# Kernel tuning notes

Measured on AMD Instinct MI355X. Metric: run time of the kernel, lower is better.

Reference implementation:

```python
import jax, jax.numpy as jnp
import numpy as np
import math

DROPOUT_P = 0.1

def setup_inputs() -> dict:
    key = jax.random.key(0)
    k1, k2, k3 = jax.random.split(key, 3)
    B, Lq, Lk, D = 8, 2048, 2048, 128
    x1 = jax.random.normal(k1, (B, Lq, D), dtype=jnp.float32)
    x2 = jax.random.normal(k2, (B, Lk, D), dtype=jnp.float32)
    qm = jnp.zeros((1, Lq, Lk), dtype=jnp.float32)  # additive attention mask
    u = jax.random.uniform(k3, (B, Lq, Lk), dtype=jnp.float32)  # dropout uniforms
    return {"x1": x1, "x2": x2, "qm": qm, "u": u}

def reference(x1, x2, qm, u):
    # scaled dot-product attention with additive mask + inverted dropout
    scale = 1.0 / math.sqrt(x1.shape[-1])
    qk = jnp.einsum('bqd,bkd->bqk', x1, x2) * scale + qm  # [B, Lq, Lk]
    attn = jax.nn.softmax(qk, axis=-1)
    keep = (u >= DROPOUT_P).astype(attn.dtype) / (1.0 - DROPOUT_P)
    attn = attn * keep
    out = jnp.einsum('bqk,bkd->bqd', attn, x2)  # [B, Lq, D]
    return out
```

## Files before the change

kernel.cpp:

```cpp
#include <hip/hip_runtime.h>
#include <hip/hip_bf16.h>
#include <stdint.h>

#define LQ 2048
#define LK 2048
#define DH 128
#define BQ 32
#define NT 16
#define LOG2E 1.44269504088896340736f
#define QSCALE 0.088388347648318447f

typedef __attribute__((ext_vector_type(8)))  short bf16x8;
typedef __attribute__((ext_vector_type(16))) float f32x16;
typedef __attribute__((ext_vector_type(4)))  float f32x4;

union FragAB { uint32_t u[4]; bf16x8 v; };

__device__ __forceinline__ uint32_t pack2_bf16(float lo, float hi) {
  union { __hip_bfloat16 b; uint16_t u; } a, c;
  a.b = __float2bfloat16(lo);
  c.b = __float2bfloat16(hi);
  return (uint32_t)a.u | ((uint32_t)c.u << 16);
}

__global__ __launch_bounds__(256)
void prep_kernel(const float* __restrict__ x2, uint16_t* __restrict__ Kp,
                 uint16_t* __restrict__ Vp) {
  __shared__ uint16_t tl[128][130];
  const int b = blockIdx.x & 7, tile = blockIdx.x >> 3;
  const int t = threadIdx.x;
  const int row0 = t >> 1, half = t & 1;

  const float* src = x2 + ((size_t)(b * 2048 + tile * 128 + row0)) * 128 + half * 64;
  uint32_t wbuf[32];
#pragma unroll
  for (int i = 0; i < 16; ++i) {
    f32x4 v = *(const f32x4*)(src + i * 4);
    wbuf[2 * i]     = pack2_bf16(v.x, v.y);
    wbuf[2 * i + 1] = pack2_bf16(v.z, v.w);
  }
  uint16_t* kdst = Kp + ((size_t)(b * 2048 + tile * 128 + row0)) * 128 + half * 64;
#pragma unroll
  for (int i = 0; i < 8; ++i)
    *(uint4*)(kdst + i * 8) = *(const uint4*)&wbuf[i * 4];
#pragma unroll
  for (int i = 0; i < 32; ++i)
    *(uint32_t*)&tl[row0][half * 64 + 2 * i] = wbuf[i];
  __syncthreads();

  const int d = t >> 1, halfk = t & 1;
  uint32_t vw[32];
#pragma unroll
  for (int i = 0; i < 32; ++i) {
    const int k = halfk * 64 + 2 * i;
    vw[i] = (uint32_t)tl[k][d] | ((uint32_t)tl[k + 1][d] << 16);
  }
  uint16_t* vdst = Vp + ((size_t)(b * 128 + d)) * 2048 + tile * 128 + halfk * 64;
#pragma unroll
  for (int i = 0; i < 8; ++i)
    *(uint4*)(vdst + i * 8) = *(const uint4*)&vw[i * 4];
}

__global__ __launch_bounds__(256)
void qmt_kernel(const float* __restrict__ qm, uint16_t* __restrict__ qmt2) {
  const int kc = threadIdx.x & 63;
  const int q  = blockIdx.x * 4 + (threadIdx.x >> 6);
  f32x4 r[8];
  const float* src = qm + (size_t)q * 2048 + kc * 32;
#pragma unroll
  for (int c = 0; c < 8; ++c) r[c] = *(const f32x4*)(src + c * 4);
#pragma unroll
  for (int h = 0; h < 2; ++h) {
    uint32_t w[8];
#pragma unroll
    for (int i = 0; i < 8; ++i) {
      const int gi0 = 2 * i, gi1 = 2 * i + 1;
      const float v0 = r[h + (gi0 >> 2) * 2][gi0 & 3] * LOG2E;
      const float v1 = r[h + (gi1 >> 2) * 2][gi1 & 3] * LOG2E;
      w[i] = pack2_bf16(v0, v1);
    }
    uint16_t* dst = qmt2 + ((size_t)(kc * 2 + h) * 2048 + q) * 16;
    uint4 lo = {w[0], w[1], w[2], w[3]};
    uint4 hi = {w[4], w[5], w[6], w[7]};
    *(uint4*)dst = lo;
    *(uint4*)(dst + 8) = hi;
  }
}

__global__ __launch_bounds__(256, 2)
void fattn_kernel(const float* __restrict__ x1,
                  const uint16_t* __restrict__ Kp,
                  const uint16_t* __restrict__ Vp,
                  const float* __restrict__ uu,
                  const uint16_t* __restrict__ qmt2,
                  float* __restrict__ out)
{
  __shared__ float scr[4][4224];

  const int tid  = threadIdx.x;
  const int ks   = tid >> 6;
  const int lane = tid & 63;
  const int ln   = lane & 31;
  const int h    = lane >> 5;

  const int b     = blockIdx.x & 7;
  const int qblk  = blockIdx.x >> 3;
  const int qbase = qblk * BQ;
  const int qrow  = qbase + ln;

  FragAB qf[8];
  {
    const float* qp = x1 + ((size_t)(b * LQ + qrow)) * DH + h * 8;
    const float qs = QSCALE * LOG2E;
#pragma unroll
    for (int dc = 0; dc < 8; ++dc) {
      f32x4 a = *(const f32x4*)(qp + dc * 16);
      f32x4 c = *(const f32x4*)(qp + dc * 16 + 4);
      qf[dc].u[0] = pack2_bf16(a.x * qs, a.y * qs);
      qf[dc].u[1] = pack2_bf16(a.z * qs, a.w * qs);
      qf[dc].u[2] = pack2_bf16(c.x * qs, c.y * qs);
      qf[dc].u[3] = pack2_bf16(c.z * qs, c.w * qs);
    }
  }

  const uint16_t* Kb = Kp + (size_t)(b * 2048 + ks * 512) * 128;
  const uint16_t* Vb = Vp + (size_t)b * 128 * 2048 + ks * 512;
  const float*    ub = uu + ((size_t)(b * LQ + qbase + h)) * LK + ks * 512 + ln;

  float ucur[16];
#pragma unroll
  for (int i = 0; i < 16; ++i)
    ucur[i] = __builtin_nontemporal_load(ub + (size_t)(2 * i) * LK);

  uint4 qc0, qc1;
  {
    const uint16_t* qp16 = qmt2 + (((size_t)(ks * 16) * 2 + h) * 2048 + qrow) * 16;
    qc0 = *(const uint4*)qp16;
    qc1 = *(const uint4*)(qp16 + 8);
  }

  float m_run = -1e30f, l_run = 0.f;
  f32x16 acco[4];
#pragma unroll
  for (int d2 = 0; d2 < 4; ++d2)
#pragma unroll
    for (int i = 0; i < 16; ++i) acco[d2][i] = 0.f;

  for (int t = 0; t < NT; ++t) {
    const uint16_t* Krow = Kb + (size_t)(t * 32 + ln) * 128 + h * 8;
    bf16x8 kf[8];
#pragma unroll
    for (int dc = 0; dc < 8; ++dc)
      kf[dc] = *(const bf16x8*)(Krow + dc * 16);

    bf16x8 vf[8];
#pragma unroll
    for (int d2 = 0; d2 < 4; ++d2)
#pragma unroll
      for (int c = 0; c < 2; ++c)
        vf[d2 * 2 + c] = *(const bf16x8*)(Vb + (size_t)(d2 * 32 + ln) * 2048 +
                                          t * 32 + c * 16 + h * 8);

    float unxt[16]; uint4 qn0, qn1;
    if (t + 1 < NT) {
#pragma unroll
      for (int i = 0; i < 16; ++i)
        unxt[i] = __builtin_nontemporal_load(ub + (t + 1) * 32 + (size_t)(2 * i) * LK);
      const uint16_t* qp16 = qmt2 + (((size_t)(ks * 16 + t + 1) * 2 + h) * 2048 + qrow) * 16;
      qn0 = *(const uint4*)qp16;
      qn1 = *(const uint4*)(qp16 + 8);
    }

    f32x16 sacc;
#pragma unroll
    for (int i = 0; i < 16; ++i) sacc[i] = 0.f;
    __builtin_amdgcn_s_setprio(1);
#pragma unroll
    for (int dc = 0; dc < 8; ++dc)
      sacc = __builtin_amdgcn_mfma_f32_32x32x16_bf16(kf[dc], qf[dc].v, sacc, 0, 0, 0);
    __builtin_amdgcn_s_setprio(0);

#define ADDQM(W, I) { sacc[I] += __uint_as_float((W) << 16); \
                      sacc[I + 1] += __uint_as_float((W) & 0xffff0000u); }
    ADDQM(qc0.x, 0)  ADDQM(qc0.y, 2)  ADDQM(qc0.z, 4)  ADDQM(qc0.w, 6)
    ADDQM(qc1.x, 8)  ADDQM(qc1.y, 10) ADDQM(qc1.z, 12) ADDQM(qc1.w, 14)
#undef ADDQM

    float pm = sacc[0];
#pragma unroll
    for (int i = 1; i < 16; ++i) pm = fmaxf(pm, sacc[i]);
    pm = fmaxf(pm, __shfl_xor(pm, 32));
    if (!__all(pm <= m_run + 8.f)) {
      const float mnew = fmaxf(m_run, pm);
      const float resc = __builtin_amdgcn_exp2f(m_run - mnew);
      l_run *= resc;
#pragma unroll
      for (int d2 = 0; d2 < 4; ++d2)
#pragma unroll
        for (int i = 0; i < 16; ++i) acco[d2][i] *= resc;
      m_run = mnew;
    }
    float rs = 0.f;
#pragma unroll
    for (int i = 0; i < 16; ++i) {
      sacc[i] = __builtin_amdgcn_exp2f(sacc[i] - m_run);
      rs += sacc[i];
    }
    rs += __shfl_xor(rs, 32);
    l_run += rs;

    uint32_t M = 0;
#pragma unroll
    for (int i = 0; i < 16; ++i) {
      unsigned long long bi = __ballot(ucur[i] >= 0.1f);
      uint32_t sel = (ln & 1) ? (uint32_t)(bi >> 32) : (uint32_t)bi;
      M = ((ln >> 1) == i) ? sel : M;
    }
#pragma unroll
    for (int g = 0; g < 4; ++g)
#pragma unroll
      for (int j2 = 0; j2 < 4; ++j2) {
        const uint32_t keep = (M >> (h * 4 + g * 8 + j2)) & 1u;
        sacc[g * 4 + j2] = keep ? sacc[g * 4 + j2] : 0.f;
      }

    uint32_t pr[4][2], sw[4][2];
#pragma unroll
    for (int g = 0; g < 4; ++g) {
      pr[g][0] = pack2_bf16(sacc[4 * g + 0], sacc[4 * g + 1]);
      pr[g][1] = pack2_bf16(sacc[4 * g + 2], sacc[4 * g + 3]);
      sw[g][0] = __shfl_xor(pr[g][0], 32);
      sw[g][1] = __shfl_xor(pr[g][1], 32);
    }
    FragAB bfr[2];
#pragma unroll
    for (int c = 0; c < 2; ++c) {
      bfr[c].u[0] = h ? sw[2 * c + 1][0] : pr[2 * c][0];
      bfr[c].u[1] = h ? sw[2 * c + 1][1] : pr[2 * c][1];
      bfr[c].u[2] = h ? pr[2 * c + 1][0] : sw[2 * c][0];
      bfr[c].u[3] = h ? pr[2 * c + 1][1] : sw[2 * c][1];
    }

    __builtin_amdgcn_s_setprio(1);
#pragma unroll
    for (int d2 = 0; d2 < 4; ++d2)
#pragma unroll
      for (int c = 0; c < 2; ++c)
        acco[d2] = __builtin_amdgcn_mfma_f32_32x32x16_bf16(vf[d2 * 2 + c], bfr[c].v,
                                                           acco[d2], 0, 0, 0);
    __builtin_amdgcn_s_setprio(0);

    if (t + 1 < NT) {
#pragma unroll
      for (int i = 0; i < 16; ++i) ucur[i] = unxt[i];
      qc0 = qn0; qc1 = qn1;
    }
  }

  float* s = scr[ks];
  s[lane]      = m_run;
  s[64 + lane] = l_run;
#pragma unroll
  for (int d2 = 0; d2 < 4; ++d2)
#pragma unroll
    for (int g = 0; g < 4; ++g) {
      f32x4 vv;
#pragma unroll
      for (int j2 = 0; j2 < 4; ++j2) vv[j2] = acco[d2][g * 4 + j2];
      *(f32x4*)(s + 128 + (size_t)(d2 * 4 + g) * 256 + lane * 4) = vv;
    }
  __syncthreads();

  {
    const float ms0 = scr[0][lane], ms1 = scr[1][lane];
    const float ms2 = scr[2][lane], ms3 = scr[3][lane];
    const float ls0 = scr[0][64 + lane], ls1 = scr[1][64 + lane];
    const float ls2 = scr[2][64 + lane], ls3 = scr[3][64 + lane];
    const float mM = fmaxf(fmaxf(ms0, ms1), fmaxf(ms2, ms3));
    const float e0 = __builtin_amdgcn_exp2f(ms0 - mM);
    const float e1 = __builtin_amdgcn_exp2f(ms1 - mM);
    const float e2 = __builtin_amdgcn_exp2f(ms2 - mM);
    const float e3 = __builtin_amdgcn_exp2f(ms3 - mM);
    const float lM = e0 * ls0 + e1 * ls1 + e2 * ls2 + e3 * ls3;
    const float inv = (1.0f / 0.9f) / lM;
    float* op = out + ((size_t)(b * LQ + qbase + ln)) * DH;
    const int d2 = ks;
#pragma unroll
    for (int g = 0; g < 4; ++g) {
      const size_t off = 128 + (size_t)(d2 * 4 + g) * 256 + lane * 4;
      f32x4 a4 = e0 * *(const f32x4*)(scr[0] + off)
               + e1 * *(const f32x4*)(scr[1] + off)
               + e2 * *(const f32x4*)(scr[2] + off)
               + e3 * *(const f32x4*)(scr[3] + off);
      a4 = a4 * inv;
      *(f32x4*)(op + d2 * 32 + 8 * g + 4 * h) = a4;
    }
  }
}

extern "C" void kernel_launch(void* const* d_in, const int* in_sizes, int n_in,
                              void* d_out, int out_size, void* d_ws, size_t ws_size,
                              hipStream_t stream) {
  (void)in_sizes; (void)n_in; (void)out_size; (void)ws_size;
  const float* x1 = (const float*)d_in[0];
  const float* x2 = (const float*)d_in[1];
  const float* qm = (const float*)d_in[2];
  const float* u  = (const float*)d_in[3];
  float* out = (float*)d_out;

  uint16_t* qmt2 = (uint16_t*)d_ws;
  uint16_t* Kp   = (uint16_t*)((char*)d_ws + (8u  << 20));
  uint16_t* Vp   = (uint16_t*)((char*)d_ws + (12u << 20));

  prep_kernel<<<dim3(128), dim3(256), 0, stream>>>(x2, Kp, Vp);
  qmt_kernel<<<dim3(512), dim3(256), 0, stream>>>(qm, qmt2);
  fattn_kernel<<<dim3(512), dim3(256), 0, stream>>>(x1, Kp, Vp, u, qmt2, out);
}
```

Measured before the change: 273.0 us.

## Precompute dropout keep-bitmasks into LDS with coalesced loads, shrink merge scratch

Before the main loop, each wave streams its 32x512 slice of dropout uniforms with coalesced 16-byte loads and ballots them into packed bitmasks stored in LDS. Per tile, the mask is rebuilt from LDS with bit-spreading, which replaces the per-tile strided scalar loads, register prefetch buffers and per-tile ballots. The cross-wave merge scratch is cut roughly in half and done in two rounds with extra barriers, lowering LDS use, presumably so more blocks fit per CU. The cost is an upfront load phase that is not overlapped with compute, plus extra synchronisation during the merge.

```diff
diff --git a/kernel.cpp b/kernel.cpp
--- a/kernel.cpp
+++ b/kernel.cpp
@@ -21,6 +21,13 @@
   a.b = __float2bfloat16(lo);
   c.b = __float2bfloat16(hi);
   return (uint32_t)a.u | ((uint32_t)c.u << 16);
+}
+
+__device__ __forceinline__ uint32_t spread4(uint32_t x) {
+  x = (x | (x << 12)) & 0x000F000Fu;
+  x = (x | (x << 6))  & 0x03030303u;
+  x = (x | (x << 3))  & 0x11111111u;
+  return x;
 }
 
 __global__ __launch_bounds__(256)
@@ -95,7 +102,9 @@
                   const uint16_t* __restrict__ qmt2,
                   float* __restrict__ out)
 {
-  __shared__ float scr[4][4224];
+  __shared__ uint32_t balLds[4 * 32 * 18];
+  __shared__ float    ml[2][4][64];
+  __shared__ f32x4    mscr[4][2][4][64];
 
   const int tid  = threadIdx.x;
   const int ks   = tid >> 6;
@@ -107,6 +116,28 @@
   const int qblk  = blockIdx.x >> 3;
   const int qbase = qblk * BQ;
   const int qrow  = qbase + ln;
+
+  uint32_t* bal = balLds + ks * 32 * 18;
+  {
+    const float* up0 = uu + ((size_t)(b * 2048 + qbase)) * 2048 + ks * 512;
+#pragma unroll 2
+    for (int r = 0; r < 32; ++r) {
+      const float* rp = up0 + (size_t)r * 2048;
+#pragma unroll
+      for (int cw = 0; cw < 2; ++cw) {
+        f32x4 v = __builtin_nontemporal_load((const f32x4*)(rp + cw * 256 + lane * 4));
+        unsigned long long b0 = __ballot(v.x >= 0.1f);
+        unsigned long long b1 = __ballot(v.y >= 0.1f);
+        unsigned long long b2 = __ballot(v.z >= 0.1f);
+        unsigned long long b3 = __ballot(v.w >= 0.1f);
+        if (lane < 4) {
+          unsigned long long bb = (lane == 0) ? b0 : (lane == 1) ? b1
+                                : (lane == 2) ? b2 : b3;
+          *(unsigned long long*)(bal + r * 18 + cw * 8 + lane * 2) = bb;
+        }
+      }
+    }
+  }
 
   FragAB qf[8];
   {
@@ -125,12 +156,6 @@
 
   const uint16_t* Kb = Kp + (size_t)(b * 2048 + ks * 512) * 128;
   const uint16_t* Vb = Vp + (size_t)b * 128 * 2048 + ks * 512;
-  const float*    ub = uu + ((size_t)(b * LQ + qbase + h)) * LK + ks * 512 + ln;
-
-  float ucur[16];
-#pragma unroll
-  for (int i = 0; i < 16; ++i)
-    ucur[i] = __builtin_nontemporal_load(ub + (size_t)(2 * i) * LK);
 
   uint4 qc0, qc1;
   {
@@ -161,11 +186,22 @@
         vf[d2 * 2 + c] = *(const bf16x8*)(Vb + (size_t)(d2 * 32 + ln) * 2048 +
                                           t * 32 + c * 16 + h * 8);
 
-    float unxt[16]; uint4 qn0, qn1;
+    uint32_t M;
+    {
+      const int cw = t >> 3, L0 = (t & 7) * 8;
+      const uint32_t* bp = bal + ln * 18 + cw * 8;
+      unsigned long long B0 = *(const unsigned long long*)(bp + 0);
+      unsigned long long B1 = *(const unsigned long long*)(bp + 2);
+      unsigned long long B2 = *(const unsigned long long*)(bp + 4);
+      unsigned long long B3 = *(const unsigned long long*)(bp + 6);
+      M = spread4((uint32_t)(B0 >> L0) & 0xFFu)
+        | (spread4((uint32_t)(B1 >> L0) & 0xFFu) << 1)
+        | (spread4((uint32_t)(B2 >> L0) & 0xFFu) << 2)
+        | (spread4((uint32_t)(B3 >> L0) & 0xFFu) << 3);
+    }
+
+    uint4 qn0, qn1;
     if (t + 1 < NT) {
-#pragma unroll
-      for (int i = 0; i < 16; ++i)
-        unxt[i] = __builtin_nontemporal_load(ub + (t + 1) * 32 + (size_t)(2 * i) * LK);
       const uint16_t* qp16 = qmt2 + (((size_t)(ks * 16 + t + 1) * 2 + h) * 2048 + qrow) * 16;
       qn0 = *(const uint4*)qp16;
       qn1 = *(const uint4*)(qp16 + 8);
@@ -209,13 +245,6 @@
     rs += __shfl_xor(rs, 32);
     l_run += rs;
 
-    uint32_t M = 0;
-#pragma unroll
-    for (int i = 0; i < 16; ++i) {
-      unsigned long long bi = __ballot(ucur[i] >= 0.1f);
-      uint32_t sel = (ln & 1) ? (uint32_t)(bi >> 32) : (uint32_t)bi;
-      M = ((ln >> 1) == i) ? sel : M;
-    }
 #pragma unroll
     for (int g = 0; g < 4; ++g)
 #pragma unroll
@@ -250,48 +279,62 @@
                                                            acco[d2], 0, 0, 0);
     __builtin_amdgcn_s_setprio(0);
 
-    if (t + 1 < NT) {
-#pragma unroll
-      for (int i = 0; i < 16; ++i) ucur[i] = unxt[i];
-      qc0 = qn0; qc1 = qn1;
-    }
-  }
-
-  float* s = scr[ks];
-  s[lane]      = m_run;
-  s[64 + lane] = l_run;
-#pragma unroll
-  for (int d2 = 0; d2 < 4; ++d2)
+    if (t + 1 < NT) { qc0 = qn0; qc1 = qn1; }
+  }
+
+  ml[0][ks][lane] = m_run;
+  ml[1][ks][lane] = l_run;
+#pragma unroll
+  for (int dd = 0; dd < 2; ++dd)
 #pragma unroll
     for (int g = 0; g < 4; ++g) {
       f32x4 vv;
 #pragma unroll
-      for (int j2 = 0; j2 < 4; ++j2) vv[j2] = acco[d2][g * 4 + j2];
-      *(f32x4*)(s + 128 + (size_t)(d2 * 4 + g) * 256 + lane * 4) = vv;
+      for (int j2 = 0; j2 < 4; ++j2) vv[j2] = acco[dd][g * 4 + j2];
+      mscr[ks][dd][g][lane] = vv;
     }
   __syncthreads();
 
+  float e0, e1, e2, e3, inv;
   {
-    const float ms0 = scr[0][lane], ms1 = scr[1][lane];
-    const float ms2 = scr[2][lane], ms3 = scr[3][lane];
-    const float ls0 = scr[0][64 + lane], ls1 = scr[1][64 + lane];
-    const float ls2 = scr[2][64 + lane], ls3 = scr[3][64 + lane];
+    const float ms0 = ml[0][0][lane], ms1 = ml[0][1][lane];
+    const float ms2 = ml[0][2][lane], ms3 = ml[0][3][lane];
+    const float ls0 = ml[1][0][lane], ls1 = ml[1][1][lane];
+    const float ls2 = ml[1][2][lane], ls3 = ml[1][3][lane];
     const float mM = fmaxf(fmaxf(ms0, ms1), fmaxf(ms2, ms3));
-    const float e0 = __builtin_amdgcn_exp2f(ms0 - mM);
-    const float e1 = __builtin_amdgcn_exp2f(ms1 - mM);
-    const float e2 = __builtin_amdgcn_exp2f(ms2 - mM);
-    const float e3 = __builtin_amdgcn_exp2f(ms3 - mM);
+    e0 = __builtin_amdgcn_exp2f(ms0 - mM);
+    e1 = __builtin_amdgcn_exp2f(ms1 - mM);
+    e2 = __builtin_amdgcn_exp2f(ms2 - mM);
+    e3 = __builtin_amdgcn_exp2f(ms3 - mM);
     const float lM = e0 * ls0 + e1 * ls1 + e2 * ls2 + e3 * ls3;
-    const float inv = (1.0f / 0.9f) / lM;
-    float* op = out + ((size_t)(b * LQ + qbase + ln)) * DH;
-    const int d2 = ks;
-#pragma unroll
-    for (int g = 0; g < 4; ++g) {
-      const size_t off = 128 + (size_t)(d2 * 4 + g) * 256 + lane * 4;
-      f32x4 a4 = e0 * *(const f32x4*)(scr[0] + off)
-               + e1 * *(const f32x4*)(scr[1] + off)
-               + e2 * *(const f32x4*)(scr[2] + off)
-               + e3 * *(const f32x4*)(scr[3] + off);
+    inv = (1.0f / 0.9f) / lM;
+  }
+
+  float* op = out + ((size_t)(b * LQ + qbase + ln)) * DH;
+  const int mydd = ks & 1;
+  const int g0   = (ks >> 1) * 2;
+
+#pragma unroll
+  for (int r = 0; r < 2; ++r) {
+    if (r == 1) {
+      __syncthreads();
+#pragma unroll
+      for (int dd = 0; dd < 2; ++dd)
+#pragma unroll
+        for (int g = 0; g < 4; ++g) {
+          f32x4 vv;
+#pragma unroll
+          for (int j2 = 0; j2 < 4; ++j2) vv[j2] = acco[2 + dd][g * 4 + j2];
+          mscr[ks][dd][g][lane] = vv;
+        }
+      __syncthreads();
+    }
+    const int d2 = 2 * r + mydd;
+#pragma unroll
+    for (int gi = 0; gi < 2; ++gi) {
+      const int g = g0 + gi;
+      f32x4 a4 = e0 * mscr[0][mydd][g][lane] + e1 * mscr[1][mydd][g][lane]
+               + e2 * mscr[2][mydd][g][lane] + e3 * mscr[3][mydd][g][lane];
       a4 = a4 * inv;
       *(f32x4*)(op + d2 * 32 + 8 * g + 4 * h) = a4;
     }
```

After: 294.5 us. 1.08x slower.

## Precompute dropout bitmask in separate kernel and split keys across 8 waves

Applied to the files above, without the earlier changes.

A new kernel reads the fp32 dropout uniforms once and packs them into per-tile 32-bit keep masks, so the attention kernel loads one word per lane per tile instead of sixteen floats plus ballots. The attention block grows to 512 threads (8 waves), each covering 256 keys, and the final cross-wave softmax merge is done in four LDS rounds. The mask layout is reorganised to be contiguous per query block. This adds an extra pass over the uniform tensor and more merge synchronisation in exchange for less traffic and less ALU work in the main loop.

```diff
diff --git a/kernel.cpp b/kernel.cpp
--- a/kernel.cpp
+++ b/kernel.cpp
@@ -6,7 +6,7 @@
 #define LK 2048
 #define DH 128
 #define BQ 32
-#define NT 16
+#define NT 8
 #define LOG2E 1.44269504088896340736f
 #define QSCALE 0.088388347648318447f
 
@@ -21,6 +21,34 @@
   a.b = __float2bfloat16(lo);
   c.b = __float2bfloat16(hi);
   return (uint32_t)a.u | ((uint32_t)c.u << 16);
+}
+
+__global__ __launch_bounds__(256)
+void mask_kernel(const float* __restrict__ uu, uint32_t* __restrict__ maskb) {
+  const int lane = threadIdx.x & 63;
+  const int wid  = blockIdx.x * 4 + (threadIdx.x >> 6);
+#pragma unroll 1
+  for (int i = 0; i < 16; ++i) {
+    const size_t F = ((size_t)i * 8192 + wid) * 256;
+    float u0 = uu[F + 0 * 64 + lane];
+    float u1 = uu[F + 1 * 64 + lane];
+    float u2 = uu[F + 2 * 64 + lane];
+    float u3 = uu[F + 3 * 64 + lane];
+    unsigned long long B0 = __ballot(u0 >= 0.1f);
+    unsigned long long B1 = __ballot(u1 >= 0.1f);
+    unsigned long long B2 = __ballot(u2 >= 0.1f);
+    unsigned long long B3 = __ballot(u3 >= 0.1f);
+    if (lane < 8) {
+      const int m = lane;
+      unsigned long long bb = (m < 2) ? B0 : (m < 4) ? B1 : (m < 6) ? B2 : B3;
+      uint32_t val = (m & 1) ? (uint32_t)(bb >> 32) : (uint32_t)bb;
+      const int row = (int)(F >> 11);
+      const int c   = (int)((F >> 5) & 63) + m;
+      const int bq  = row >> 5;
+      const int ln  = row & 31;
+      maskb[((size_t)bq * 64 + c) * 32 + ln] = val;
+    }
+  }
 }
 
 __global__ __launch_bounds__(256)
@@ -62,7 +90,7 @@
 }
 
 __global__ __launch_bounds__(256)
-void qmt_kernel(const float* __restrict__ qm, uint16_t* __restrict__ qmt2) {
+void qmt_kernel(const float* __restrict__ qm, uint16_t* __restrict__ qmt3) {
   const int kc = threadIdx.x & 63;
   const int q  = blockIdx.x * 4 + (threadIdx.x >> 6);
   f32x4 r[8];
@@ -79,7 +107,7 @@
       const float v1 = r[h + (gi1 >> 2) * 2][gi1 & 3] * LOG2E;
       w[i] = pack2_bf16(v0, v1);
     }
-    uint16_t* dst = qmt2 + ((size_t)(kc * 2 + h) * 2048 + q) * 16;
+    uint16_t* dst = qmt3 + (((size_t)(q >> 5) * 64 + kc) * 2 + h) * 512 + (q & 31) * 16;
     uint4 lo = {w[0], w[1], w[2], w[3]};
     uint4 hi = {w[4], w[5], w[6], w[7]};
     *(uint4*)dst = lo;
@@ -87,15 +115,16 @@
   }
 }
 
-__global__ __launch_bounds__(256, 2)
+__global__ __launch_bounds__(512, 4)
 void fattn_kernel(const float* __restrict__ x1,
                   const uint16_t* __restrict__ Kp,
                   const uint16_t* __restrict__ Vp,
-                  const float* __restrict__ uu,
-                  const uint16_t* __restrict__ qmt2,
+                  const uint32_t* __restrict__ maskb,
+                  const uint16_t* __restrict__ qmt3,
                   float* __restrict__ out)
 {
-  __shared__ float scr[4][4224];
+  __shared__ float ml[2][8][64];
+  __shared__ f32x4 mscr[8][4][64];
 
   const int tid  = threadIdx.x;
   const int ks   = tid >> 6;
@@ -123,18 +152,15 @@
     }
   }
 
-  const uint16_t* Kb = Kp + (size_t)(b * 2048 + ks * 512) * 128;
-  const uint16_t* Vb = Vp + (size_t)b * 128 * 2048 + ks * 512;
-  const float*    ub = uu + ((size_t)(b * LQ + qbase + h)) * LK + ks * 512 + ln;
-
-  float ucur[16];
-#pragma unroll
-  for (int i = 0; i < 16; ++i)
-    ucur[i] = __builtin_nontemporal_load(ub + (size_t)(2 * i) * LK);
-
+  const uint16_t* Kb = Kp + (size_t)(b * 2048 + ks * 256) * 128;
+  const uint16_t* Vb = Vp + (size_t)b * 128 * 2048 + ks * 256;
+  const uint32_t* mb = maskb + ((size_t)(b * 64 + qblk) * 64 + ks * 8) * 32 + ln;
+  const uint16_t* qmb = qmt3 + ((size_t)(qblk * 64 + ks * 8) * 2) * 512 + ln * 16;
+
+  uint32_t M = mb[0];
   uint4 qc0, qc1;
   {
-    const uint16_t* qp16 = qmt2 + (((size_t)(ks * 16) * 2 + h) * 2048 + qrow) * 16;
+    const uint16_t* qp16 = qmb + h * 512;
     qc0 = *(const uint4*)qp16;
     qc1 = *(const uint4*)(qp16 + 8);
   }
@@ -161,12 +187,10 @@
         vf[d2 * 2 + c] = *(const bf16x8*)(Vb + (size_t)(d2 * 32 + ln) * 2048 +
                                           t * 32 + c * 16 + h * 8);
 
-    float unxt[16]; uint4 qn0, qn1;
+    uint32_t Mn = 0; uint4 qn0, qn1;
     if (t + 1 < NT) {
-#pragma unroll
-      for (int i = 0; i < 16; ++i)
-        unxt[i] = __builtin_nontemporal_load(ub + (t + 1) * 32 + (size_t)(2 * i) * LK);
-      const uint16_t* qp16 = qmt2 + (((size_t)(ks * 16 + t + 1) * 2 + h) * 2048 + qrow) * 16;
+      Mn = mb[(t + 1) * 32];
+      const uint16_t* qp16 = qmb + ((size_t)(t + 1) * 2 + h) * 512;
       qn0 = *(const uint4*)qp16;
       qn1 = *(const uint4*)(qp16 + 8);
     }
@@ -209,13 +233,6 @@
     rs += __shfl_xor(rs, 32);
     l_run += rs;
 
-    uint32_t M = 0;
-#pragma unroll
-    for (int i = 0; i < 16; ++i) {
-      unsigned long long bi = __ballot(ucur[i] >= 0.1f);
-      uint32_t sel = (ln & 1) ? (uint32_t)(bi >> 32) : (uint32_t)bi;
-      M = ((ln >> 1) == i) ? sel : M;
-    }
 #pragma unroll
     for (int g = 0; g < 4; ++g)
 #pragma unroll
@@ -250,50 +267,46 @@
                                                            acco[d2], 0, 0, 0);
     __builtin_amdgcn_s_setprio(0);
 
-    if (t + 1 < NT) {
-#pragma unroll
-      for (int i = 0; i < 16; ++i) ucur[i] = unxt[i];
-      qc0 = qn0; qc1 = qn1;
-    }
-  }
-
-  float* s = scr[ks];
-  s[lane]      = m_run;
-  s[64 + lane] = l_run;
-#pragma unroll
-  for (int d2 = 0; d2 < 4; ++d2)
+    if (t + 1 < NT) { M = Mn; qc0 = qn0; qc1 = qn1; }
+  }
+
+  ml[0][ks][lane] = m_run;
+  ml[1][ks][lane] = l_run;
+
+  float e[8], inv;
+  float* op = out + ((size_t)(b * LQ + qbase + ln)) * DH;
+
+#pragma unroll
+  for (int r = 0; r < 4; ++r) {
+    if (r) __syncthreads();
 #pragma unroll
     for (int g = 0; g < 4; ++g) {
       f32x4 vv;
 #pragma unroll
-      for (int j2 = 0; j2 < 4; ++j2) vv[j2] = acco[d2][g * 4 + j2];
-      *(f32x4*)(s + 128 + (size_t)(d2 * 4 + g) * 256 + lane * 4) = vv;
-    }
-  __syncthreads();
-
-  {
-    const float ms0 = scr[0][lane], ms1 = scr[1][lane];
-    const float ms2 = scr[2][lane], ms3 = scr[3][lane];
-    const float ls0 = scr[0][64 + lane], ls1 = scr[1][64 + lane];
-    const float ls2 = scr[2][64 + lane], ls3 = scr[3][64 + lane];
-    const float mM = fmaxf(fmaxf(ms0, ms1), fmaxf(ms2, ms3));
-    const float e0 = __builtin_amdgcn_exp2f(ms0 - mM);
-    const float e1 = __builtin_amdgcn_exp2f(ms1 - mM);
-    const float e2 = __builtin_amdgcn_exp2f(ms2 - mM);
-    const float e3 = __builtin_amdgcn_exp2f(ms3 - mM);
-    const float lM = e0 * ls0 + e1 * ls1 + e2 * ls2 + e3 * ls3;
-    const float inv = (1.0f / 0.9f) / lM;
-    float* op = out + ((size_t)(b * LQ + qbase + ln)) * DH;
-    const int d2 = ks;
-#pragma unroll
-    for (int g = 0; g < 4; ++g) {
-      const size_t off = 128 + (size_t)(d2 * 4 + g) * 256 + lane * 4;
-      f32x4 a4 = e0 * *(const f32x4*)(scr[0] + off)
-               + e1 * *(const f32x4*)(scr[1] + off)
-               + e2 * *(const f32x4*)(scr[2] + off)
-               + e3 * *(const f32x4*)(scr[3] + off);
+      for (int j2 = 0; j2 < 4; ++j2) vv[j2] = acco[r][g * 4 + j2];
+      mscr[ks][g][lane] = vv;
+    }
+    __syncthreads();
+
+    if (r == 0) {
+      float mM = -1e30f;
+#pragma unroll
+      for (int k = 0; k < 8; ++k) mM = fmaxf(mM, ml[0][k][lane]);
+      float lM = 0.f;
+#pragma unroll
+      for (int k = 0; k < 8; ++k) {
+        e[k] = __builtin_amdgcn_exp2f(ml[0][k][lane] - mM);
+        lM += e[k] * ml[1][k][lane];
+      }
+      inv = (1.0f / 0.9f) / lM;
+    }
+
+    if (ks < 4) {
+      f32x4 a4 = {0.f, 0.f, 0.f, 0.f};
+#pragma unroll
+      for (int k = 0; k < 8; ++k) a4 += e[k] * mscr[k][ks][lane];
       a4 = a4 * inv;
-      *(f32x4*)(op + d2 * 32 + 8 * g + 4 * h) = a4;
+      *(f32x4*)(op + r * 32 + 8 * ks + 4 * h) = a4;
     }
   }
 }
@@ -308,11 +321,13 @@
   const float* u  = (const float*)d_in[3];
   float* out = (float*)d_out;
 
-  uint16_t* qmt2 = (uint16_t*)d_ws;
-  uint16_t* Kp   = (uint16_t*)((char*)d_ws + (8u  << 20));
-  uint16_t* Vp   = (uint16_t*)((char*)d_ws + (12u << 20));
-
+  uint16_t* qmt3  = (uint16_t*)d_ws;
+  uint16_t* Kp    = (uint16_t*)((char*)d_ws + (8u  << 20));
+  uint16_t* Vp    = (uint16_t*)((char*)d_ws + (12u << 20));
+  uint32_t* maskb = (uint32_t*)((char*)d_ws + (16u << 20));
+
+  mask_kernel<<<dim3(2048), dim3(256), 0, stream>>>(u, maskb);
   prep_kernel<<<dim3(128), dim3(256), 0, stream>>>(x2, Kp, Vp);
-  qmt_kernel<<<dim3(512), dim3(256), 0, stream>>>(qm, qmt2);
-  fattn_kernel<<<dim3(512), dim3(256), 0, stream>>>(x1, Kp, Vp, u, qmt2, out);
-}
+  qmt_kernel<<<dim3(512), dim3(256), 0, stream>>>(qm, qmt3);
+  fattn_kernel<<<dim3(512), dim3(512), 0, stream>>>(x1, Kp, Vp, maskb, qmt3, out);
+}
```

New measurement: 432.7 us. +58.5%, slower.
